# Optimization experiments

Measured on AMD Instinct MI355X. Metric: run time of the kernel, lower is better.

The kernel has to match this reference:

```python
import jax, jax.numpy as jnp
import numpy as np

N_NODES = 50000
EMBED_DIM = 512
N_EDGES = 800000
NEG_SLOPE = 0.01  # nn.LeakyReLU default


def setup_inputs() -> dict:
    key = jax.random.key(0)
    k1, k2, k3 = jax.random.split(key, 3)
    X = jax.random.normal(k1, (N_NODES, EMBED_DIM), dtype=jnp.float32)
    # Glorot-ish scale for the GCNConv weight
    W = jax.random.normal(k2, (EMBED_DIM, EMBED_DIM), dtype=jnp.float32) / np.sqrt(EMBED_DIM)
    b = jnp.zeros((EMBED_DIM,), dtype=jnp.float32)
    edge_index = jax.random.randint(k3, (2, N_EDGES), 0, N_NODES, dtype=jnp.int32)
    return {"X": X, "W": W, "b": b, "edge_index": edge_index}


def reference(X, W, b, edge_index):
    N = X.shape[0]
    # GCNConv: add self-loops, symmetric normalization deg^-1/2 A deg^-1/2
    loop = jnp.arange(N, dtype=edge_index.dtype)
    src = jnp.concatenate([edge_index[0], loop])  # [E+N]
    dst = jnp.concatenate([edge_index[1], loop])  # [E+N]
    deg = jax.ops.segment_sum(jnp.ones_like(dst, dtype=X.dtype), dst, num_segments=N)
    dinv = jnp.where(deg > 0, jax.lax.rsqrt(deg), 0.0)  # deg^{-1/2}, inf->0
    norm = dinv[src] * dinv[dst]                         # [E+N]
    H = X @ W                                            # [N, D] dense GEMM
    msgs = H[src] * norm[:, None]                        # [E+N, D] gathered messages
    out = jax.ops.segment_sum(msgs, dst, num_segments=N) + b
    # LeakyReLU activation; Dropout is identity in eval mode
    return jnp.where(out >= 0, out, NEG_SLOPE * out)
```

## Files before the change

kernel.cpp:

```cpp
#include <hip/hip_runtime.h>
#include <cstdint>
#include <cstddef>

#define DFEAT 512
#define BM 128
#define BN 128
#define BK 32

typedef __attribute__((ext_vector_type(8))) short bf16x8;
typedef __attribute__((ext_vector_type(4))) float f32x4;

#define GLOBAL_AS __attribute__((address_space(1)))
#define LDS_AS __attribute__((address_space(3)))

__device__ __forceinline__ unsigned short f2bf(float f) {
  unsigned u = __float_as_uint(f);
  u = u + 0x7fffu + ((u >> 16) & 1u);
  return (unsigned short)(u >> 16);
}

__device__ __forceinline__ float bf2f_lo(unsigned u) { return __uint_as_float(u << 16); }
__device__ __forceinline__ float bf2f_hi(unsigned u) { return __uint_as_float(u & 0xffff0000u); }

__device__ __forceinline__ void gl_lds16(const void* g, void* l) {
  __builtin_amdgcn_global_load_lds((const GLOBAL_AS unsigned int*)g,
                                   (LDS_AS unsigned int*)l, 16, 0, 0);
}

__global__ void k_countcast(const int* __restrict__ dst, int* __restrict__ deg8,
                            int E, int N,
                            const float* __restrict__ X, unsigned short* __restrict__ Xb,
                            int total8) {
  const int b = blockIdx.x;
  const int m = b % 5;
  if (m == 4) {
    const int i = (b / 5) * 256 + threadIdx.x;
    if (i < E) {
      const int d = __builtin_nontemporal_load(dst + i);
      atomicAdd(&deg8[(size_t)(b & 7) * N + d], 1);
    }
    return;
  }
  const int i = ((b / 5) * 4 + m) * 256 + threadIdx.x;
  if (i >= total8) return;
  const f32x4 a = __builtin_nontemporal_load(reinterpret_cast<const f32x4*>(X + (size_t)i * 8));
  const f32x4 c = __builtin_nontemporal_load(reinterpret_cast<const f32x4*>(X + (size_t)i * 8 + 4));
  uint4 o;
  o.x = (unsigned)f2bf(a[0]) | ((unsigned)f2bf(a[1]) << 16);
  o.y = (unsigned)f2bf(a[2]) | ((unsigned)f2bf(a[3]) << 16);
  o.z = (unsigned)f2bf(c[0]) | ((unsigned)f2bf(c[1]) << 16);
  o.w = (unsigned)f2bf(c[2]) | ((unsigned)f2bf(c[3]) << 16);
  *reinterpret_cast<uint4*>(Xb + (size_t)i * 8) = o;
}

__global__ __launch_bounds__(1024) void k_scan(const int* __restrict__ deg8,
                                               int* __restrict__ deg,
                                               int* __restrict__ rowStart,
                                               int* __restrict__ fillPos, int N) {
  const int t = threadIdx.x;
  const int base = blockIdx.x * 1024;
  __shared__ int sm[1024];
  int pre = 0;
  for (int i = t; i < base; i += 1024) {
    int s = 0;
#pragma unroll
    for (int x = 0; x < 8; ++x) s += deg8[(size_t)x * N + i];
    pre += s;
  }
  sm[t] = pre;
  __syncthreads();
  for (int d = 512; d > 0; d >>= 1) {
    if (t < d) sm[t] += sm[t + d];
    __syncthreads();
  }
  const int blockBase = sm[0];
  __syncthreads();
  const int idx = base + t;
  int v = 0;
  if (idx < N) {
#pragma unroll
    for (int x = 0; x < 8; ++x) v += deg8[(size_t)x * N + idx];
    deg[idx] = v;
  }
  sm[t] = v;
  __syncthreads();
  for (int d = 1; d < 1024; d <<= 1) {
    const int o = (t >= d) ? sm[t - d] : 0;
    __syncthreads();
    sm[t] += o;
    __syncthreads();
  }
  if (idx < N) {
    const int ex = blockBase + sm[t] - v;
    rowStart[idx] = ex;
    fillPos[idx] = ex;
    if (idx == N - 1) rowStart[N] = ex + v;
  }
}

__global__ void k_fillwt(const int* __restrict__ src, const int* __restrict__ dst,
                         int* __restrict__ fillPos, int2* __restrict__ cw,
                         const int* __restrict__ deg, int E,
                         const float* __restrict__ W, unsigned short* __restrict__ Wt) {
  const int b = blockIdx.x;
  const int m = b & 3;
  if (m == 3) {
    const int i = (b >> 2) * 256 + threadIdx.x;
    if (i < DFEAT * DFEAT) {
      const int k = i >> 9, n = i & 511;
      Wt[(size_t)n * DFEAT + k] = f2bf(W[i]);
    }
    return;
  }
  const int i = ((b >> 2) * 3 + m) * 256 + threadIdx.x;
  if (i < E) {
    const int d = dst[i], s = src[i];
    const int pos = atomicAdd(&fillPos[d], 1);
    int2 q; q.x = s; q.y = __float_as_int(rsqrtf((float)(deg[s] + 1)));
    cw[pos] = q;
  }
}

template <bool TAIL>
__device__ __forceinline__ void agg8(const unsigned short* __restrict__ Xb,
                                     const int2* __restrict__ cw,
                                     int p, int e, int lane, float* acc) {
  unsigned long long q[8];
#pragma unroll
  for (int i = 0; i < 8; ++i) {
    int pi = p + i;
    if (TAIL) pi = (pi < e) ? pi : (e - 1);
    q[i] = __builtin_nontemporal_load(reinterpret_cast<const unsigned long long*>(cw + pi));
  }
  uint4 v[8];
#pragma unroll
  for (int i = 0; i < 8; ++i)
    v[i] = *reinterpret_cast<const uint4*>(Xb + (size_t)(unsigned)q[i] * DFEAT + lane * 8);
#pragma unroll
  for (int i = 0; i < 8; ++i) {
    float w = __uint_as_float((unsigned)(q[i] >> 32));
    if (TAIL) w = (p + i < e) ? w : 0.0f;
    acc[0] = fmaf(w, bf2f_lo(v[i].x), acc[0]); acc[1] = fmaf(w, bf2f_hi(v[i].x), acc[1]);
    acc[2] = fmaf(w, bf2f_lo(v[i].y), acc[2]); acc[3] = fmaf(w, bf2f_hi(v[i].y), acc[3]);
    acc[4] = fmaf(w, bf2f_lo(v[i].z), acc[4]); acc[5] = fmaf(w, bf2f_hi(v[i].z), acc[5]);
    acc[6] = fmaf(w, bf2f_lo(v[i].w), acc[6]); acc[7] = fmaf(w, bf2f_hi(v[i].w), acc[7]);
  }
}

__global__ __launch_bounds__(256) void k_aggregate(const unsigned short* __restrict__ Xb,
                                                   const int2* __restrict__ cw,
                                                   const int* __restrict__ rowStart,
                                                   unsigned short* __restrict__ Y, int N) {
  const int row = blockIdx.x * 4 + (threadIdx.x >> 6);
  const int lane = threadIdx.x & 63;
  float acc[8] = {0.f, 0.f, 0.f, 0.f, 0.f, 0.f, 0.f, 0.f};
  if (row < N) {
    const int s = rowStart[row], e = rowStart[row + 1];
    const float sc = rsqrtf((float)(e - s + 1));
    const uint4 v0 = *reinterpret_cast<const uint4*>(Xb + (size_t)row * DFEAT + lane * 8);
    acc[0] = sc * bf2f_lo(v0.x); acc[1] = sc * bf2f_hi(v0.x);
    acc[2] = sc * bf2f_lo(v0.y); acc[3] = sc * bf2f_hi(v0.y);
    acc[4] = sc * bf2f_lo(v0.z); acc[5] = sc * bf2f_hi(v0.z);
    acc[6] = sc * bf2f_lo(v0.w); acc[7] = sc * bf2f_hi(v0.w);
    int p = s;
    for (; p + 8 <= e; p += 8) agg8<false>(Xb, cw, p, e, lane, acc);
    if (p < e) agg8<true>(Xb, cw, p, e, lane, acc);
#pragma unroll
    for (int j = 0; j < 8; ++j) acc[j] *= sc;
  }
  uint4 o;
  o.x = (unsigned)f2bf(acc[0]) | ((unsigned)f2bf(acc[1]) << 16);
  o.y = (unsigned)f2bf(acc[2]) | ((unsigned)f2bf(acc[3]) << 16);
  o.z = (unsigned)f2bf(acc[4]) | ((unsigned)f2bf(acc[5]) << 16);
  o.w = (unsigned)f2bf(acc[6]) | ((unsigned)f2bf(acc[7]) << 16);
  *reinterpret_cast<uint4*>(Y + (size_t)row * DFEAT + lane * 8) = o;
}

__global__ __launch_bounds__(256) void k_gemm(const unsigned short* __restrict__ Y,
                                              const unsigned short* __restrict__ Wt,
                                              const float* __restrict__ bias,
                                              float* __restrict__ out, int M) {
  __shared__ unsigned short As[BM * BK];
  __shared__ unsigned short Bs[BN * BK];
  const int tid = threadIdx.x;
  const int lane = tid & 63;
  const int wave = tid >> 6;
  const int l16 = lane & 15;
  const int quad = lane >> 4;
  const int wm = (wave >> 1) * 64;
  const int wn = (wave & 1) * 64;

  const int nwg = gridDim.x;
  const int q8 = nwg >> 3, r8 = nwg & 7;
  const int xcd = blockIdx.x & 7, loc = blockIdx.x >> 3;
  const int wg = (xcd < r8 ? xcd * (q8 + 1) : r8 * (q8 + 1) + (xcd - r8) * q8) + loc;
  const int m0 = (wg >> 2) * BM;
  const int n0 = (wg & 3) * BN;

  f32x4 acc[4][4];
#pragma unroll
  for (int mi = 0; mi < 4; ++mi)
#pragma unroll
    for (int ni = 0; ni < 4; ++ni) { f32x4 z = {0.f, 0.f, 0.f, 0.f}; acc[mi][ni] = z; }

  const int ci0 = wave * 64 + lane;
  const int ci1 = 256 + ci0;
  const int ra0 = ci0 >> 2, ka0 = (((ci0 & 3) - (ra0 >> 1)) & 3) * 8;
  const int ra1 = ci1 >> 2, ka1 = (((ci1 & 3) - (ra1 >> 1)) & 3) * 8;

  const unsigned short* Ag0 = Y + (size_t)(m0 + ra0) * DFEAT + ka0;
  const unsigned short* Ag1 = Y + (size_t)(m0 + ra1) * DFEAT + ka1;
  const unsigned short* Bg0 = Wt + (size_t)(n0 + ra0) * DFEAT + ka0;
  const unsigned short* Bg1 = Wt + (size_t)(n0 + ra1) * DFEAT + ka1;
  unsigned short* La0 = As + ci0 * 8;
  unsigned short* La1 = As + ci1 * 8;
  unsigned short* Lb0 = Bs + ci0 * 8;
  unsigned short* Lb1 = Bs + ci1 * 8;

  const int rotA = (quad + ((wm + l16) >> 1)) & 3;
  const int rotB = (quad + ((wn + l16) >> 1)) & 3;
  const unsigned short* AsRd = As + (wm + l16) * BK + rotA * 8;
  const unsigned short* BsRd = Bs + (wn + l16) * BK + rotB * 8;

  for (int kk = 0; kk < DFEAT; kk += BK) {
    gl_lds16(Ag0 + kk, La0);
    gl_lds16(Ag1 + kk, La1);
    gl_lds16(Bg0 + kk, Lb0);
    gl_lds16(Bg1 + kk, Lb1);
    __syncthreads();
    bf16x8 av[4], bv[4];
#pragma unroll
    for (int mi = 0; mi < 4; ++mi)
      av[mi] = *reinterpret_cast<const bf16x8*>(AsRd + mi * 16 * BK);
#pragma unroll
    for (int ni = 0; ni < 4; ++ni)
      bv[ni] = *reinterpret_cast<const bf16x8*>(BsRd + ni * 16 * BK);
#pragma unroll
    for (int mi = 0; mi < 4; ++mi)
#pragma unroll
      for (int ni = 0; ni < 4; ++ni)
        acc[mi][ni] = __builtin_amdgcn_mfma_f32_16x16x32_bf16(av[mi], bv[ni], acc[mi][ni], 0, 0, 0);
    __syncthreads();
  }

  float bvals[4];
#pragma unroll
  for (int ni = 0; ni < 4; ++ni) bvals[ni] = bias[n0 + wn + 16 * ni + l16];

#pragma unroll
  for (int mi = 0; mi < 4; ++mi) {
#pragma unroll
    for (int r = 0; r < 4; ++r) {
      int row = m0 + wm + 16 * mi + quad * 4 + r;
      if (row < M) {
#pragma unroll
        for (int ni = 0; ni < 4; ++ni) {
          float v = acc[mi][ni][r] + bvals[ni];
          v = (v >= 0.f) ? v : 0.01f * v;
          out[(size_t)row * DFEAT + n0 + wn + 16 * ni + l16] = v;
        }
      }
    }
  }
}

extern "C" void kernel_launch(void* const* d_in, const int* in_sizes, int n_in,
                              void* d_out, int out_size, void* d_ws, size_t ws_size,
                              hipStream_t stream) {
  const float* X = (const float*)d_in[0];
  const float* W = (const float*)d_in[1];
  const float* b = (const float*)d_in[2];
  const int* ei  = (const int*)d_in[3];
  const int D = DFEAT;
  const int N = in_sizes[0] / D;
  const int E = in_sizes[3] / 2;
  const int* src = ei;
  const int* dst = ei + E;
  float* out = (float*)d_out;

  uintptr_t p = (uintptr_t)d_ws;
  auto carve = [&](size_t bytes) -> void* {
    uintptr_t r = p;
    p += (bytes + 255) & ~(size_t)255;
    return (void*)r;
  };
  int*   deg8     = (int*)carve(sizeof(int) * (size_t)N * 8);
  int*   deg      = (int*)carve(sizeof(int) * (size_t)N);
  int*   rowStart = (int*)carve(sizeof(int) * (size_t)(N + 1));
  int*   fillPos  = (int*)carve(sizeof(int) * (size_t)N);
  int2*  cw       = (int2*)carve(sizeof(int2) * (size_t)E);
  unsigned short* Wt = (unsigned short*)carve(sizeof(unsigned short) * (size_t)D * D);
  const int Mtiles = (N + BM - 1) / BM;
  const int Mpad = Mtiles * BM;
  unsigned short* Y  = (unsigned short*)carve(sizeof(unsigned short) * (size_t)Mpad * D);

  unsigned short* Xb = (unsigned short*)d_out;

  const int total8 = N * D / 8;
  const int fb = (E + 255) / 256;
  const int xb = (total8 + 255) / 256;
  const int wb = (D * D + 255) / 256;

  const int xq = (xb + 3) / 4;
  const int nA = 5 * (fb > xq ? fb : xq);
  const int fq = (fb + 2) / 3;
  const int nB = 4 * (fq > wb ? fq : wb);

  hipMemsetAsync(deg8, 0, sizeof(int) * (size_t)N * 8, stream);
  hipLaunchKernelGGL(k_countcast, dim3(nA), dim3(256), 0, stream,
                     dst, deg8, E, N, X, Xb, total8);
  hipLaunchKernelGGL(k_scan,      dim3((N + 1023) / 1024), dim3(1024), 0, stream,
                     deg8, deg, rowStart, fillPos, N);
  hipLaunchKernelGGL(k_fillwt,    dim3(nB), dim3(256), 0, stream,
                     src, dst, fillPos, cw, deg, E, W, Wt);
  hipLaunchKernelGGL(k_aggregate, dim3(Mpad / 4), dim3(256), 0, stream,
                     Xb, cw, rowStart, Y, N);
  hipLaunchKernelGGL(k_gemm,      dim3(Mtiles * 4), dim3(256), 0, stream, Y, Wt, b, out, N);
}
```

Measured before the change: 413.5 us.

## Split X cast across countcast and scan kernels; halve feature width per aggregate block

The fp32-to-bf16 cast of X is split so half runs alongside the degree count and the other half runs as extra blocks of the scan kernel, filling its otherwise tiny grid. The aggregate kernel now has each block process 256 of the 512 features with 8-byte gathers, doubling the grid. Blocks for the two halves of the same rows are placed next to each other so cache reuse is preserved. This aims to balance work across the front kernels and raise aggregate parallelism, at the cost of reading every edge list twice and using narrower per-lane loads.

```diff
diff --git a/kernel.cpp b/kernel.cpp
--- a/kernel.cpp
+++ b/kernel.cpp
@@ -27,37 +27,50 @@
                                    (LDS_AS unsigned int*)l, 16, 0, 0);
 }
 
+__device__ __forceinline__ void cast8(const float* __restrict__ X,
+                                      unsigned short* __restrict__ Xb, int g) {
+  const f32x4 a = __builtin_nontemporal_load(reinterpret_cast<const f32x4*>(X + (size_t)g * 8));
+  const f32x4 c = __builtin_nontemporal_load(reinterpret_cast<const f32x4*>(X + (size_t)g * 8 + 4));
+  uint4 o;
+  o.x = (unsigned)f2bf(a[0]) | ((unsigned)f2bf(a[1]) << 16);
+  o.y = (unsigned)f2bf(a[2]) | ((unsigned)f2bf(a[3]) << 16);
+  o.z = (unsigned)f2bf(c[0]) | ((unsigned)f2bf(c[1]) << 16);
+  o.w = (unsigned)f2bf(c[2]) | ((unsigned)f2bf(c[3]) << 16);
+  *reinterpret_cast<uint4*>(Xb + (size_t)g * 8) = o;
+}
+
 __global__ void k_countcast(const int* __restrict__ dst, int* __restrict__ deg8,
                             int E, int N,
                             const float* __restrict__ X, unsigned short* __restrict__ Xb,
-                            int total8) {
+                            int castA8) {
   const int b = blockIdx.x;
-  const int m = b % 5;
-  if (m == 4) {
-    const int i = (b / 5) * 256 + threadIdx.x;
+  const int m = b % 3;
+  if (m == 2) {
+    const int i = (b / 3) * 256 + threadIdx.x;
     if (i < E) {
       const int d = __builtin_nontemporal_load(dst + i);
       atomicAdd(&deg8[(size_t)(b & 7) * N + d], 1);
     }
     return;
   }
-  const int i = ((b / 5) * 4 + m) * 256 + threadIdx.x;
-  if (i >= total8) return;
-  const f32x4 a = __builtin_nontemporal_load(reinterpret_cast<const f32x4*>(X + (size_t)i * 8));
-  const f32x4 c = __builtin_nontemporal_load(reinterpret_cast<const f32x4*>(X + (size_t)i * 8 + 4));
-  uint4 o;
-  o.x = (unsigned)f2bf(a[0]) | ((unsigned)f2bf(a[1]) << 16);
-  o.y = (unsigned)f2bf(a[2]) | ((unsigned)f2bf(a[3]) << 16);
-  o.z = (unsigned)f2bf(c[0]) | ((unsigned)f2bf(c[1]) << 16);
-  o.w = (unsigned)f2bf(c[2]) | ((unsigned)f2bf(c[3]) << 16);
-  *reinterpret_cast<uint4*>(Xb + (size_t)i * 8) = o;
-}
-
-__global__ __launch_bounds__(1024) void k_scan(const int* __restrict__ deg8,
-                                               int* __restrict__ deg,
-                                               int* __restrict__ rowStart,
-                                               int* __restrict__ fillPos, int N) {
+  const int g = ((b / 3) * 2 + m) * 256 + threadIdx.x;
+  if (g < castA8) cast8(X, Xb, g);
+}
+
+__global__ __launch_bounds__(1024) void k_scancast(const int* __restrict__ deg8,
+                                                   int* __restrict__ deg,
+                                                   int* __restrict__ rowStart,
+                                                   int* __restrict__ fillPos, int N,
+                                                   const float* __restrict__ X,
+                                                   unsigned short* __restrict__ Xb,
+                                                   int castA8, int total8) {
+  const int SB = (N + 1023) >> 10;
   const int t = threadIdx.x;
+  if (blockIdx.x >= SB) {
+    const int g = castA8 + (blockIdx.x - SB) * 1024 + t;
+    if (g < total8) cast8(X, Xb, g);
+    return;
+  }
   const int base = blockIdx.x * 1024;
   __shared__ int sm[1024];
   int pre = 0;
@@ -122,9 +135,9 @@
 }
 
 template <bool TAIL>
-__device__ __forceinline__ void agg8(const unsigned short* __restrict__ Xb,
-                                     const int2* __restrict__ cw,
-                                     int p, int e, int lane, float* acc) {
+__device__ __forceinline__ void agg8h(const unsigned short* __restrict__ xh,
+                                      const int2* __restrict__ cw,
+                                      int p, int e, float* acc) {
   unsigned long long q[8];
 #pragma unroll
   for (int i = 0; i < 8; ++i) {
@@ -132,18 +145,16 @@
     if (TAIL) pi = (pi < e) ? pi : (e - 1);
     q[i] = __builtin_nontemporal_load(reinterpret_cast<const unsigned long long*>(cw + pi));
   }
-  uint4 v[8];
+  uint2 v[8];
 #pragma unroll
   for (int i = 0; i < 8; ++i)
-    v[i] = *reinterpret_cast<const uint4*>(Xb + (size_t)(unsigned)q[i] * DFEAT + lane * 8);
+    v[i] = *reinterpret_cast<const uint2*>(xh + (size_t)(unsigned)q[i] * DFEAT);
 #pragma unroll
   for (int i = 0; i < 8; ++i) {
     float w = __uint_as_float((unsigned)(q[i] >> 32));
     if (TAIL) w = (p + i < e) ? w : 0.0f;
     acc[0] = fmaf(w, bf2f_lo(v[i].x), acc[0]); acc[1] = fmaf(w, bf2f_hi(v[i].x), acc[1]);
     acc[2] = fmaf(w, bf2f_lo(v[i].y), acc[2]); acc[3] = fmaf(w, bf2f_hi(v[i].y), acc[3]);
-    acc[4] = fmaf(w, bf2f_lo(v[i].z), acc[4]); acc[5] = fmaf(w, bf2f_hi(v[i].z), acc[5]);
-    acc[6] = fmaf(w, bf2f_lo(v[i].w), acc[6]); acc[7] = fmaf(w, bf2f_hi(v[i].w), acc[7]);
   }
 }
 
@@ -151,29 +162,29 @@
                                                    const int2* __restrict__ cw,
                                                    const int* __restrict__ rowStart,
                                                    unsigned short* __restrict__ Y, int N) {
-  const int row = blockIdx.x * 4 + (threadIdx.x >> 6);
+  const int b7 = blockIdx.x & 7;
+  const int half = b7 >> 2;
+  const int rq = (blockIdx.x >> 3) * 4 + (b7 & 3);
+  const int row = rq * 4 + (threadIdx.x >> 6);
   const int lane = threadIdx.x & 63;
-  float acc[8] = {0.f, 0.f, 0.f, 0.f, 0.f, 0.f, 0.f, 0.f};
+  const unsigned short* xh = Xb + half * 256 + lane * 4;
+  float acc[4] = {0.f, 0.f, 0.f, 0.f};
   if (row < N) {
     const int s = rowStart[row], e = rowStart[row + 1];
     const float sc = rsqrtf((float)(e - s + 1));
-    const uint4 v0 = *reinterpret_cast<const uint4*>(Xb + (size_t)row * DFEAT + lane * 8);
+    const uint2 v0 = *reinterpret_cast<const uint2*>(xh + (size_t)row * DFEAT);
     acc[0] = sc * bf2f_lo(v0.x); acc[1] = sc * bf2f_hi(v0.x);
     acc[2] = sc * bf2f_lo(v0.y); acc[3] = sc * bf2f_hi(v0.y);
-    acc[4] = sc * bf2f_lo(v0.z); acc[5] = sc * bf2f_hi(v0.z);
-    acc[6] = sc * bf2f_lo(v0.w); acc[7] = sc * bf2f_hi(v0.w);
     int p = s;
-    for (; p + 8 <= e; p += 8) agg8<false>(Xb, cw, p, e, lane, acc);
-    if (p < e) agg8<true>(Xb, cw, p, e, lane, acc);
-#pragma unroll
-    for (int j = 0; j < 8; ++j) acc[j] *= sc;
-  }
-  uint4 o;
+    for (; p + 8 <= e; p += 8) agg8h<false>(xh, cw, p, e, acc);
+    if (p < e) agg8h<true>(xh, cw, p, e, acc);
+#pragma unroll
+    for (int j = 0; j < 4; ++j) acc[j] *= sc;
+  }
+  uint2 o;
   o.x = (unsigned)f2bf(acc[0]) | ((unsigned)f2bf(acc[1]) << 16);
   o.y = (unsigned)f2bf(acc[2]) | ((unsigned)f2bf(acc[3]) << 16);
-  o.z = (unsigned)f2bf(acc[4]) | ((unsigned)f2bf(acc[5]) << 16);
-  o.w = (unsigned)f2bf(acc[6]) | ((unsigned)f2bf(acc[7]) << 16);
-  *reinterpret_cast<uint4*>(Y + (size_t)row * DFEAT + lane * 8) = o;
+  *reinterpret_cast<uint2*>(Y + (size_t)row * DFEAT + half * 256 + lane * 4) = o;
 }
 
 __global__ __launch_bounds__(256) void k_gemm(const unsigned short* __restrict__ Y,
@@ -297,23 +308,25 @@
   unsigned short* Xb = (unsigned short*)d_out;
 
   const int total8 = N * D / 8;
-  const int fb = (E + 255) / 256;
-  const int xb = (total8 + 255) / 256;
+  const int cb = (E + 255) / 256;
+  const int castA8 = ((total8 / 2) + 255) & ~255;
+  const int castAb = castA8 / 256;
+  const int nA = 3 * (cb > (castAb + 1) / 2 ? cb : (castAb + 1) / 2);
+  const int SB = (N + 1023) / 1024;
+  const int nBcast = (total8 - castA8 + 1023) / 1024;
+  const int fb = cb;
+  const int fq = (fb + 2) / 3;
   const int wb = (D * D + 255) / 256;
-
-  const int xq = (xb + 3) / 4;
-  const int nA = 5 * (fb > xq ? fb : xq);
-  const int fq = (fb + 2) / 3;
-  const int nB = 4 * (fq > wb ? fq : wb);
+  const int nC = 4 * (fq > wb ? fq : wb);
 
   hipMemsetAsync(deg8, 0, sizeof(int) * (size_t)N * 8, stream);
   hipLaunchKernelGGL(k_countcast, dim3(nA), dim3(256), 0, stream,
-                     dst, deg8, E, N, X, Xb, total8);
-  hipLaunchKernelGGL(k_scan,      dim3((N + 1023) / 1024), dim3(1024), 0, stream,
-                     deg8, deg, rowStart, fillPos, N);
-  hipLaunchKernelGGL(k_fillwt,    dim3(nB), dim3(256), 0, stream,
+                     dst, deg8, E, N, X, Xb, castA8);
+  hipLaunchKernelGGL(k_scancast,  dim3(SB + nBcast), dim3(1024), 0, stream,
+                     deg8, deg, rowStart, fillPos, N, X, Xb, castA8, total8);
+  hipLaunchKernelGGL(k_fillwt,    dim3(nC), dim3(256), 0, stream,
                      src, dst, fillPos, cw, deg, E, W, Wt);
-  hipLaunchKernelGGL(k_aggregate, dim3(Mpad / 4), dim3(256), 0, stream,
+  hipLaunchKernelGGL(k_aggregate, dim3(Mpad / 2), dim3(256), 0, stream,
                      Xb, cw, rowStart, Y, N);
   hipLaunchKernelGGL(k_gemm,      dim3(Mtiles * 4), dim3(256), 0, stream, Y, Wt, b, out, N);
 }
```

After: 427.7 us. 3.4% more time.
